# Kernel tuning notes

Measured on AMD Instinct MI355X. Metric: run time of the kernel, lower is better.

## Reference

```python
import jax, jax.numpy as jnp
import numpy as np

N_MENTIONS = 4096
N_PAIRS = 32768
N_SEGMENTS = 1024  # number of spans (ragged softmax groups)
G_DIM = 3 * 768    # span representation dim (3*embed_dim)
D_IN = 3 * G_DIM + 20
HIDDEN = 150


def setup_inputs() -> dict:
    key = jax.random.key(0)
    ks = jax.random.split(key, 11)
    inp = {
        "g_i": jax.random.normal(ks[0], (N_MENTIONS, G_DIM), jnp.float32),
        "mention_scores": jax.random.normal(ks[1], (N_MENTIONS, 1), jnp.float32),
        "speaker_embed": jax.random.normal(ks[2], (3, 20), jnp.float32) * 0.02,
        "W1": jax.random.normal(ks[3], (D_IN, HIDDEN), jnp.float32) * (1.0 / np.sqrt(D_IN)),
        "b1": jnp.zeros((HIDDEN,), jnp.float32),
        "W2": jax.random.normal(ks[4], (HIDDEN, 1), jnp.float32) * (1.0 / np.sqrt(HIDDEN)),
        "b2": jnp.zeros((1,), jnp.float32),
        "mention_ids": jax.random.randint(ks[5], (N_PAIRS,), 0, N_MENTIONS),
        "antecedent_ids": jax.random.randint(ks[6], (N_PAIRS,), 0, N_MENTIONS),
        "speaker_labels": jax.random.randint(ks[7], (N_PAIRS,), 0, 3),
        "segment_ids": jnp.sort(jax.random.randint(ks[8], (N_PAIRS,), 0, N_SEGMENTS)),
    }
    return inp


def reference(g_i, mention_scores, speaker_embed, W1, b1, W2, b2,
              mention_ids, antecedent_ids, speaker_labels, segment_ids):
    # Gather mention / antecedent span representations. [P, G]
    i_g = g_i[mention_ids]
    j_g = g_i[antecedent_ids]
    phi = speaker_embed[speaker_labels]  # [P, speaker_dim]

    # Pair features: cat(i_g, j_g, i_g*j_g, phi). [P, D_IN]
    pairs = jnp.concatenate([i_g, j_g, i_g * j_g, phi], axis=1)

    # Score MLP: Linear -> ReLU -> Linear(->1). (dropout off in eval)
    h = jax.nn.relu(pairs @ W1 + b1)          # [P, HIDDEN]
    s_ij = (h @ W2 + b2)[:, 0]                # [P]

    # coref score = s_i + s_j + s_ij
    s_i = mention_scores[mention_ids, 0]
    s_j = mention_scores[antecedent_ids, 0]
    scores = s_i + s_j + s_ij                 # [P]

    # Ragged per-span softmax with an appended epsilon logit of 0.0.
    seg_max = jax.ops.segment_max(scores, segment_ids, num_segments=N_SEGMENTS)
    m = jnp.maximum(seg_max, 0.0)             # include epsilon=0 in the max
    e = jnp.exp(scores - m[segment_ids])      # [P]
    eps_e = jnp.exp(-m)                       # [S] exp(0 - m)
    denom = jax.ops.segment_sum(e, segment_ids, num_segments=N_SEGMENTS) + eps_e
    pair_probs = e / denom[segment_ids]       # [P]
    eps_probs = eps_e / denom                 # [S]

    # Flattened: all pair probs followed by the per-span epsilon probs.
    return jnp.concatenate([pair_probs, eps_probs])
```

## Files before the change

kernel.cpp:

```cpp
#include <hip/hip_runtime.h>
#include <cstdint>

#define NM   4096
#define NP   32768
#define NSEG 1024
#define GD   2304
#define HID  150
#define NPAD 160
#define KG32 72
#define SEG_ELEMS (KG32 * 10 * 512)

typedef unsigned short u16;
typedef short s16x8 __attribute__((ext_vector_type(8)));
typedef float f32x4 __attribute__((ext_vector_type(4)));
typedef uint32_t u32x4 __attribute__((ext_vector_type(4)));

union Frag {
    uint32_t u[4];
    s16x8    v;
};

__device__ inline uint32_t cvtpk(float lo, float hi) {
    uint32_t r;
    asm("v_cvt_pk_bf16_f32 %0, %1, %2" : "=v"(r) : "v"(lo), "v"(hi));
    return r;
}

__device__ inline f32x4 mfma16(s16x8 a, s16x8 b, f32x4 c) {
    return __builtin_amdgcn_mfma_f32_16x16x32_bf16(a, b, c, 0, 0, 0);
}

__device__ inline s16x8 prodpack(u32x4 iu, u32x4 ju) {
    Frag f;
#pragma unroll
    for (int m = 0; m < 4; ++m) {
        uint32_t x = iu[m], y = ju[m];
        float lo = __builtin_bit_cast(float, x << 16) *
                   __builtin_bit_cast(float, y << 16);
        float hi = __builtin_bit_cast(float, x & 0xffff0000u) *
                   __builtin_bit_cast(float, y & 0xffff0000u);
        f.u[m] = cvtpk(lo, hi);
    }
    return f.v;
}

__global__ void prep_pack_kernel(const float* __restrict__ W1,
                                 u16* __restrict__ wpack) {
    int idx = blockIdx.x * 256 + threadIdx.x;
    if (idx >= 3 * KG32 * 10 * 64) return;
    int lane = idx & 63;
    int t    = idx >> 6;
    int nf   = t % 10;
    int sk   = t / 10;
    int seg  = sk / KG32, kg = sk % KG32;
    int kbase = (seg == 0) ? 2 * GD : ((seg == 1) ? 0 : GD);
    int n    = nf * 16 + (lane & 15);
    int krow = kbase + kg * 32 + ((lane >> 4) << 3);
    u32x4 d = (u32x4){0u, 0u, 0u, 0u};
    if (n < HID) {
#pragma unroll
        for (int jj = 0; jj < 4; ++jj) {
            float v0 = W1[(size_t)(krow + 2 * jj) * HID + n];
            float v1 = W1[(size_t)(krow + 2 * jj + 1) * HID + n];
            d[jj] = cvtpk(v0, v1);
        }
    }
    *(u32x4*)(wpack + (size_t)idx * 8) = d;
}

__global__ __launch_bounds__(1024)
void prep_sort_kernel(const float* __restrict__ spk,
                      const float* __restrict__ W1,
                      const float* __restrict__ b1,
                      const float* __restrict__ W2,
                      const int* __restrict__ mids,
                      float* __restrict__ phib,
                      float* __restrict__ w2pad,
                      int* __restrict__ perm) {
    __shared__ int cnt[NM];
    __shared__ int bas[NM];
    __shared__ int lsum[1024];

    const int t = threadIdx.x;

    if (t < 3 * NPAD) {
        int s = t / NPAD, n = t - s * NPAD;
        float a = 0.f;
        if (n < HID) {
            for (int d = 0; d < 20; ++d)
                a = fmaf(spk[s * 20 + d], W1[(size_t)(3 * GD + d) * HID + n], a);
            a += b1[n];
        }
        phib[t] = a;
    } else if (t < 4 * NPAD) {
        int n = t - 3 * NPAD;
        w2pad[n] = (n < HID) ? W2[n] : 0.f;
    }

#pragma unroll
    for (int j = 0; j < 4; ++j) cnt[t + j * 1024] = 0;
    __syncthreads();

    for (int p = t; p < NP; p += 1024) atomicAdd(&cnt[mids[p]], 1);
    __syncthreads();

    int v[4];
    int s = 0;
#pragma unroll
    for (int j = 0; j < 4; ++j) { v[j] = cnt[4 * t + j]; s += v[j]; }
    int val = s;
    lsum[t] = val;
    __syncthreads();
    for (int off = 1; off < 1024; off <<= 1) {
        int x = (t >= off) ? lsum[t - off] : 0;
        __syncthreads();
        val += x;
        lsum[t] = val;
        __syncthreads();
    }
    int run = val - s;
#pragma unroll
    for (int j = 0; j < 4; ++j) {
        bas[4 * t + j] = run;
        run += v[j];
        cnt[4 * t + j] = 0;
    }
    __syncthreads();

    for (int p = t; p < NP; p += 1024) {
        int m = mids[p];
        int pos = bas[m] + atomicAdd(&cnt[m], 1);
        perm[pos] = p;
    }
}

struct A2 { f32x4 x0, x1; };

__launch_bounds__(256)
__global__ void gemm_pre_kernel(const float* __restrict__ gi,
                                const u16* __restrict__ wpackIJ,
                                u16* __restrict__ gbf,
                                float* __restrict__ APre) {
    const int tid = threadIdx.x;
    const int kh = tid >> 6, lane = tid & 63;
    const int quad = lane >> 4, l15 = lane & 15;
    const int mt = blockIdx.x, ng = blockIdx.y;
    const u16* wp = wpackIJ + (size_t)ng * SEG_ELEMS + lane * 8;
    const int row = mt * 16 + l15;

    __shared__ float xch[3][64][44];

    f32x4 acc[10];
#pragma unroll
    for (int b = 0; b < 10; ++b) acc[b] = (f32x4){0.f, 0.f, 0.f, 0.f};

    const float* ap = gi + (size_t)row * GD + quad * 8;
    u16* gb = gbf + (size_t)row * GD + quad * 8;
    const bool emit = (ng == 0);
    const int u0 = kh * 18;

    A2 a0, a1, a2;
    Frag b0[10], b1[10];

#define LDA(ax, k) { ax.x0 = *(const f32x4*)(ap + (u0 + (k)) * 32); \
                     ax.x1 = *(const f32x4*)(ap + (u0 + (k)) * 32 + 4); }
#define LDBP(bb, k) { const u16* wn = wp + (size_t)(u0 + (k)) * 5120; \
        _Pragma("unroll") for (int nf = 0; nf < 10; ++nf) \
            bb[nf].v = *(const s16x8*)(const void*)(wn + nf * 512); }
#define PHP(k, ax, bb) { \
        Frag a; \
        a.u[0] = cvtpk(ax.x0[0], ax.x0[1]); a.u[1] = cvtpk(ax.x0[2], ax.x0[3]); \
        a.u[2] = cvtpk(ax.x1[0], ax.x1[1]); a.u[3] = cvtpk(ax.x1[2], ax.x1[3]); \
        if (emit) *(u32x4*)(gb + (u0 + (k)) * 32) = *(const u32x4*)a.u; \
        _Pragma("unroll") for (int nf = 0; nf < 10; ++nf) \
            acc[nf] = mfma16(a.v, bb[nf].v, acc[nf]); }

    LDBP(b0, 0); LDBP(b1, 1);
    LDA(a0, 0); LDA(a1, 1); LDA(a2, 2);

#pragma unroll 1
    for (int t = 0; t < 2; ++t) {
        const int kb = t * 6;
        PHP(kb + 0, a0, b0); LDBP(b0, kb + 2); LDA(a0, kb + 3);
        PHP(kb + 1, a1, b1); LDBP(b1, kb + 3); LDA(a1, kb + 4);
        PHP(kb + 2, a2, b0); LDBP(b0, kb + 4); LDA(a2, kb + 5);
        PHP(kb + 3, a0, b1); LDBP(b1, kb + 5); LDA(a0, kb + 6);
        PHP(kb + 4, a1, b0); LDBP(b0, kb + 6); LDA(a1, kb + 7);
        PHP(kb + 5, a2, b1); LDBP(b1, kb + 7); LDA(a2, kb + 8);
    }
    PHP(12, a0, b0); LDBP(b0, 14); LDA(a0, 15);
    PHP(13, a1, b1); LDBP(b1, 15); LDA(a1, 16);
    PHP(14, a2, b0); LDBP(b0, 16); LDA(a2, 17);
    PHP(15, a0, b1); LDBP(b1, 17);
    PHP(16, a1, b0);
    PHP(17, a2, b1);

#undef LDA
#undef LDBP
#undef PHP

    if (kh != 0) {
        float* dst = &xch[kh - 1][lane][0];
#pragma unroll
        for (int nf = 0; nf < 10; ++nf)
            *(f32x4*)(dst + nf * 4) = acc[nf];
    }
    __syncthreads();
    if (kh == 0) {
#pragma unroll
        for (int k = 0; k < 3; ++k) {
            const float* src = &xch[k][lane][0];
#pragma unroll
            for (int nf = 0; nf < 10; ++nf)
                acc[nf] += *(const f32x4*)(src + nf * 4);
        }
        const int colbase = ng * NPAD + l15;
        float* Ap = APre + (size_t)(mt * 16 + quad * 4) * 320 + colbase;
#pragma unroll
        for (int nf = 0; nf < 10; ++nf)
#pragma unroll
            for (int r = 0; r < 4; ++r)
                Ap[(size_t)r * 320 + nf * 16] = acc[nf][r];
    }
}

struct G4 { u32x4 i0, j0, i1, j1; };

__launch_bounds__(128)
__global__ void gemm_pairs_kernel(const u16* __restrict__ gbf,
                                  const u16* __restrict__ wpackP,
                                  const float* __restrict__ APre,
                                  const float* __restrict__ phib,
                                  const float* __restrict__ w2pad,
                                  const float* __restrict__ mscore,
                                  const float* __restrict__ b2,
                                  const int* __restrict__ mids,
                                  const int* __restrict__ aids,
                                  const int* __restrict__ slab,
                                  const int* __restrict__ perm,
                                  float* __restrict__ scores) {
    const int tid = threadIdx.x;
    const int wave = tid >> 6, lane = tid & 63;
    const int quad = lane >> 4, l15 = lane & 15;
    const int base = blockIdx.x * 64 + wave * 32;

    f32x4 acc[2][10];
#pragma unroll
    for (int a = 0; a < 2; ++a)
#pragma unroll
        for (int b = 0; b < 10; ++b) acc[a][b] = (f32x4){0.f, 0.f, 0.f, 0.f};

    const int p0 = perm[base + l15], p1 = perm[base + 16 + l15];
    const u16* ip0 = gbf + (size_t)mids[p0] * GD + quad * 8;
    const u16* jp0 = gbf + (size_t)aids[p0] * GD + quad * 8;
    const u16* ip1 = gbf + (size_t)mids[p1] * GD + quad * 8;
    const u16* jp1 = gbf + (size_t)aids[p1] * GD + quad * 8;
    const u16* wl = wpackP + lane * 8;

    G4 g0, g1, g2;
    Frag b0[10], b1[10];

#define LDG(g, k) { const int off = (k) * 32; \
        g.i0 = *(const u32x4*)(ip0 + off); g.j0 = *(const u32x4*)(jp0 + off); \
        g.i1 = *(const u32x4*)(ip1 + off); g.j1 = *(const u32x4*)(jp1 + off); }
#define LDB(bb, k) { const u16* wn = wl + (size_t)(k) * 5120; \
        _Pragma("unroll") for (int nf = 0; nf < 10; ++nf) \
            bb[nf].v = *(const s16x8*)(const void*)(wn + nf * 512); }
#define PH(g, bb) { \
        s16x8 a0 = prodpack(g.i0, g.j0); \
        s16x8 a1 = prodpack(g.i1, g.j1); \
        _Pragma("unroll") for (int nf = 0; nf < 10; ++nf) { \
            acc[0][nf] = mfma16(a0, bb[nf].v, acc[0][nf]); \
            acc[1][nf] = mfma16(a1, bb[nf].v, acc[1][nf]); } }

    LDG(g0, 0); LDG(g1, 1); LDG(g2, 2);
    LDB(b0, 0); LDB(b1, 1);

#pragma unroll 1
    for (int t = 0; t < 11; ++t) {
        const int kb = t * 6;
        PH(g0, b0); LDG(g0, kb + 3); LDB(b0, kb + 2);
        PH(g1, b1); LDG(g1, kb + 4); LDB(b1, kb + 3);
        PH(g2, b0); LDG(g2, kb + 5); LDB(b0, kb + 4);
        PH(g0, b1); LDG(g0, kb + 6); LDB(b1, kb + 5);
        PH(g1, b0); LDG(g1, kb + 7); LDB(b0, kb + 6);
        PH(g2, b1); LDG(g2, kb + 8); LDB(b1, kb + 7);
    }
    PH(g0, b0); LDG(g0, 69); LDB(b0, 68);
    PH(g1, b1); LDG(g1, 70); LDB(b1, 69);
    PH(g2, b0); LDG(g2, 71); LDB(b0, 70);
    PH(g0, b1); LDB(b1, 71);
    PH(g1, b0);
    PH(g2, b1);

#undef LDG
#undef LDB
#undef PH

    float w2v[10];
#pragma unroll
    for (int nf = 0; nf < 10; ++nf) w2v[nf] = w2pad[nf * 16 + l15];
    const float b2v = b2[0];

#pragma unroll
    for (int mf = 0; mf < 2; ++mf)
#pragma unroll
        for (int r = 0; r < 4; ++r) {
            const int p  = perm[base + mf * 16 + quad * 4 + r];
            const int mi = mids[p], ai = aids[p], sp = slab[p];
            const float* Ai = APre + (size_t)mi * 320;
            const float* Bj = APre + (size_t)ai * 320 + NPAD;
            const float* Ph = phib + sp * NPAD;
            float partial = 0.f;
#pragma unroll
            for (int nf = 0; nf < 10; ++nf) {
                const int c = nf * 16 + l15;
                float h = acc[mf][nf][r] + Ai[c] + Bj[c] + Ph[c];
                h = fmaxf(h, 0.f);
                partial = fmaf(h, w2v[nf], partial);
            }
            partial += __shfl_xor(partial, 1);
            partial += __shfl_xor(partial, 2);
            partial += __shfl_xor(partial, 4);
            partial += __shfl_xor(partial, 8);
            if (l15 == 0)
                scores[p] = partial + b2v + mscore[mi] + mscore[ai];
        }
}

__global__ void seg_softmax_kernel(const float* __restrict__ scores,
                                   const int* __restrict__ seg,
                                   float* __restrict__ out) {
    const int s = blockIdx.x;
    const int lane = threadIdx.x;
    int lo = 0, hi = NP;
    while (lo < hi) { int mid = (lo + hi) >> 1; if (seg[mid] < s) lo = mid + 1; else hi = mid; }
    const int start = lo;
    int lo2 = start, hi2 = NP;
    while (lo2 < hi2) { int mid = (lo2 + hi2) >> 1; if (seg[mid] <= s) lo2 = mid + 1; else hi2 = mid; }
    const int end = lo2;

    float m = 0.f;
    for (int i = start + lane; i < end; i += 64) m = fmaxf(m, scores[i]);
#pragma unroll
    for (int msk = 1; msk < 64; msk <<= 1) m = fmaxf(m, __shfl_xor(m, msk));

    float sum = 0.f;
    for (int i = start + lane; i < end; i += 64) sum += __expf(scores[i] - m);
#pragma unroll
    for (int msk = 1; msk < 64; msk <<= 1) sum += __shfl_xor(sum, msk);

    const float epse = __expf(-m);
    const float inv  = 1.f / (sum + epse);
    for (int i = start + lane; i < end; i += 64) out[i] = __expf(scores[i] - m) * inv;
    if (lane == 0) out[NP + s] = epse * inv;
}

extern "C" void kernel_launch(void* const* d_in, const int* in_sizes, int n_in,
                              void* d_out, int out_size, void* d_ws, size_t ws_size,
                              hipStream_t stream) {
    const float* gi     = (const float*)d_in[0];
    const float* mscore = (const float*)d_in[1];
    const float* spk    = (const float*)d_in[2];
    const float* W1     = (const float*)d_in[3];
    const float* b1     = (const float*)d_in[4];
    const float* W2     = (const float*)d_in[5];
    const float* b2     = (const float*)d_in[6];
    const int*   mids   = (const int*)d_in[7];
    const int*   aids   = (const int*)d_in[8];
    const int*   slab   = (const int*)d_in[9];
    const int*   segs   = (const int*)d_in[10];
    float* out = (float*)d_out;

    char* w = (char*)d_ws;
    u16*   gbf    = (u16*)w;
    u16*   wpack  = (u16*)(w + 18874368);
    float* APre   = (float*)(w + 21086208);
    float* scores = (float*)(w + 26329088);
    float* phib   = (float*)(w + 26460160);
    float* w2pad  = (float*)(w + 26462080);
    int*   perm   = (int*)(w + 26462720);

    prep_pack_kernel<<<dim3((3 * KG32 * 10 * 64 + 255) / 256), dim3(256), 0, stream>>>(W1, wpack);
    prep_sort_kernel<<<dim3(1), dim3(1024), 0, stream>>>(spk, W1, b1, W2, mids,
                                                         phib, w2pad, perm);
    gemm_pre_kernel<<<dim3(256, 2), dim3(256), 0, stream>>>(gi, wpack + SEG_ELEMS, gbf, APre);
    gemm_pairs_kernel<<<dim3(512), dim3(128), 0, stream>>>(gbf, wpack, APre, phib, w2pad,
                                                           mscore, b2, mids, aids, slab,
                                                           perm, scores);
    seg_softmax_kernel<<<dim3(NSEG), dim3(64), 0, stream>>>(scores, segs, out);
}
```

Before: 224.8 us.

## Split single-block counting sort across grid and fuse into pack and GEMM kernels

The one-block prep_sort kernel, which did the mention-id histogram, scan and scatter serially on 1024 threads, is broken up. The histogram now runs as global atomics in extra blocks of a merged pack/phi prep kernel. A small kernel keeps only the scan, and the scatter into perm runs as 128 extra blocks appended to gemm_pre_kernel. This removes a serial single-CU bottleneck but adds a memset launch and global atomics.

```diff
diff --git a/kernel.cpp b/kernel.cpp
--- a/kernel.cpp
+++ b/kernel.cpp
@@ -44,66 +44,62 @@
     return f.v;
 }
 
-__global__ void prep_pack_kernel(const float* __restrict__ W1,
-                                 u16* __restrict__ wpack) {
-    int idx = blockIdx.x * 256 + threadIdx.x;
-    if (idx >= 3 * KG32 * 10 * 64) return;
-    int lane = idx & 63;
-    int t    = idx >> 6;
-    int nf   = t % 10;
-    int sk   = t / 10;
-    int seg  = sk / KG32, kg = sk % KG32;
-    int kbase = (seg == 0) ? 2 * GD : ((seg == 1) ? 0 : GD);
-    int n    = nf * 16 + (lane & 15);
-    int krow = kbase + kg * 32 + ((lane >> 4) << 3);
-    u32x4 d = (u32x4){0u, 0u, 0u, 0u};
-    if (n < HID) {
-#pragma unroll
-        for (int jj = 0; jj < 4; ++jj) {
-            float v0 = W1[(size_t)(krow + 2 * jj) * HID + n];
-            float v1 = W1[(size_t)(krow + 2 * jj + 1) * HID + n];
-            d[jj] = cvtpk(v0, v1);
+__launch_bounds__(256)
+__global__ void prep_kernel(const float* __restrict__ W1,
+                            const float* __restrict__ spk,
+                            const float* __restrict__ b1,
+                            const float* __restrict__ W2,
+                            const int* __restrict__ mids,
+                            u16* __restrict__ wpack,
+                            float* __restrict__ phib,
+                            float* __restrict__ w2pad,
+                            int* __restrict__ cnt) {
+    const int b = blockIdx.x;
+    if (b < 540) {
+        int idx = b * 256 + threadIdx.x;
+        int lane = idx & 63;
+        int t    = idx >> 6;
+        int nf   = t % 10;
+        int sk   = t / 10;
+        int seg  = sk / KG32, kg = sk % KG32;
+        int kbase = (seg == 0) ? 2 * GD : ((seg == 1) ? 0 : GD);
+        int n    = nf * 16 + (lane & 15);
+        int krow = kbase + kg * 32 + ((lane >> 4) << 3);
+        u32x4 d = (u32x4){0u, 0u, 0u, 0u};
+        if (n < HID) {
+#pragma unroll
+            for (int jj = 0; jj < 4; ++jj) {
+                float v0 = W1[(size_t)(krow + 2 * jj) * HID + n];
+                float v1 = W1[(size_t)(krow + 2 * jj + 1) * HID + n];
+                d[jj] = cvtpk(v0, v1);
+            }
         }
-    }
-    *(u32x4*)(wpack + (size_t)idx * 8) = d;
+        *(u32x4*)(wpack + (size_t)idx * 8) = d;
+    } else if (b < 543) {
+        int t = (b - 540) * 256 + threadIdx.x;
+        if (t < 3 * NPAD) {
+            int s = t / NPAD, n = t - s * NPAD;
+            float a = 0.f;
+            if (n < HID) {
+                for (int d = 0; d < 20; ++d)
+                    a = fmaf(spk[s * 20 + d], W1[(size_t)(3 * GD + d) * HID + n], a);
+                a += b1[n];
+            }
+            phib[t] = a;
+        } else if (t < 4 * NPAD) {
+            int n = t - 3 * NPAD;
+            w2pad[n] = (n < HID) ? W2[n] : 0.f;
+        }
+    } else {
+        int p = (b - 543) * 256 + threadIdx.x;
+        if (p < NP) atomicAdd(&cnt[mids[p]], 1);
+    }
 }
 
 __global__ __launch_bounds__(1024)
-void prep_sort_kernel(const float* __restrict__ spk,
-                      const float* __restrict__ W1,
-                      const float* __restrict__ b1,
-                      const float* __restrict__ W2,
-                      const int* __restrict__ mids,
-                      float* __restrict__ phib,
-                      float* __restrict__ w2pad,
-                      int* __restrict__ perm) {
-    __shared__ int cnt[NM];
-    __shared__ int bas[NM];
+void sort_scan_kernel(int* __restrict__ cnt, int* __restrict__ bas) {
     __shared__ int lsum[1024];
-
     const int t = threadIdx.x;
-
-    if (t < 3 * NPAD) {
-        int s = t / NPAD, n = t - s * NPAD;
-        float a = 0.f;
-        if (n < HID) {
-            for (int d = 0; d < 20; ++d)
-                a = fmaf(spk[s * 20 + d], W1[(size_t)(3 * GD + d) * HID + n], a);
-            a += b1[n];
-        }
-        phib[t] = a;
-    } else if (t < 4 * NPAD) {
-        int n = t - 3 * NPAD;
-        w2pad[n] = (n < HID) ? W2[n] : 0.f;
-    }
-
-#pragma unroll
-    for (int j = 0; j < 4; ++j) cnt[t + j * 1024] = 0;
-    __syncthreads();
-
-    for (int p = t; p < NP; p += 1024) atomicAdd(&cnt[mids[p]], 1);
-    __syncthreads();
-
     int v[4];
     int s = 0;
 #pragma unroll
@@ -125,13 +121,6 @@
         run += v[j];
         cnt[4 * t + j] = 0;
     }
-    __syncthreads();
-
-    for (int p = t; p < NP; p += 1024) {
-        int m = mids[p];
-        int pos = bas[m] + atomicAdd(&cnt[m], 1);
-        perm[pos] = p;
-    }
 }
 
 struct A2 { f32x4 x0, x1; };
@@ -140,15 +129,30 @@
 __global__ void gemm_pre_kernel(const float* __restrict__ gi,
                                 const u16* __restrict__ wpackIJ,
                                 u16* __restrict__ gbf,
-                                float* __restrict__ APre) {
+                                float* __restrict__ APre,
+                                const int* __restrict__ mids,
+                                const int* __restrict__ bas,
+                                int* __restrict__ cnt,
+                                int* __restrict__ perm) {
+    const int blk = blockIdx.x;
+    __shared__ float xch[3][64][44];
+
+    if (blk >= 512) {
+        int p = (blk - 512) * 256 + threadIdx.x;
+        if (p < NP) {
+            int m = mids[p];
+            int pos = bas[m] + atomicAdd(&cnt[m], 1);
+            perm[pos] = p;
+        }
+        return;
+    }
+
     const int tid = threadIdx.x;
     const int kh = tid >> 6, lane = tid & 63;
     const int quad = lane >> 4, l15 = lane & 15;
-    const int mt = blockIdx.x, ng = blockIdx.y;
+    const int mt = blk & 255, ng = blk >> 8;
     const u16* wp = wpackIJ + (size_t)ng * SEG_ELEMS + lane * 8;
     const int row = mt * 16 + l15;
-
-    __shared__ float xch[3][64][44];
 
     f32x4 acc[10];
 #pragma unroll
@@ -379,12 +383,16 @@
     float* scores = (float*)(w + 26329088);
     float* phib   = (float*)(w + 26460160);
     float* w2pad  = (float*)(w + 26462080);
-    int*   perm   = (int*)(w + 26462720);
-
-    prep_pack_kernel<<<dim3((3 * KG32 * 10 * 64 + 255) / 256), dim3(256), 0, stream>>>(W1, wpack);
-    prep_sort_kernel<<<dim3(1), dim3(1024), 0, stream>>>(spk, W1, b1, W2, mids,
-                                                         phib, w2pad, perm);
-    gemm_pre_kernel<<<dim3(256, 2), dim3(256), 0, stream>>>(gi, wpack + SEG_ELEMS, gbf, APre);
+    int*   cnt    = (int*)(w + 26462720);
+    int*   bas    = (int*)(w + 26479104);
+    int*   perm   = (int*)(w + 26495488);
+
+    hipMemsetAsync(cnt, 0, NM * sizeof(int), stream);
+    prep_kernel<<<dim3(671), dim3(256), 0, stream>>>(W1, spk, b1, W2, mids,
+                                                     wpack, phib, w2pad, cnt);
+    sort_scan_kernel<<<dim3(1), dim3(1024), 0, stream>>>(cnt, bas);
+    gemm_pre_kernel<<<dim3(640), dim3(256), 0, stream>>>(gi, wpack + SEG_ELEMS, gbf, APre,
+                                                         mids, bas, cnt, perm);
     gemm_pairs_kernel<<<dim3(512), dim3(128), 0, stream>>>(gbf, wpack, APre, phib, w2pad,
                                                            mscore, b2, mids, aids, slab,
                                                            perm, scores);
```

New measurement: 198.6 us. 11.6% less time.
